# Kernel tuning notes

Measured on AMD Instinct MI355X. Metric: run time of the kernel, lower is better.

The kernel has to match this reference:

```python
import jax, jax.numpy as jnp
import numpy as np

C, H, W = 3, 128, 128
N_PIX = C * H * W            # 49152
N_RET = N_PIX // 16          # 3072
N_LGN = N_RET                # 3072
N_V1 = 2 * N_RET             # 6144
N_IT = N_RET                 # 3072
N_CLS = 1000
BATCH = 256


def setup_inputs() -> dict:
    key = jax.random.key(0)
    ks = jax.random.split(key, 14)
    x = jax.random.normal(ks[0], (BATCH, C, H, W), dtype=jnp.float32)
    w_ret = jax.random.normal(ks[1], (N_RET, 16), dtype=jnp.float32) * 0.1
    b_ret = jax.random.normal(ks[2], (N_RET,), dtype=jnp.float32) * 0.1
    w_lgn = jax.random.normal(ks[3], (N_LGN, 16), dtype=jnp.float32) * 0.1
    b_lgn = jax.random.normal(ks[4], (N_LGN,), dtype=jnp.float32) * 0.1
    w_v1 = jax.random.normal(ks[5], (N_V1, 32), dtype=jnp.float32) * 0.1
    b_v1 = jax.random.normal(ks[6], (N_V1,), dtype=jnp.float32) * 0.1
    w_it = jax.random.normal(ks[7], (N_IT, 32), dtype=jnp.float32) * 0.1
    b_it = jax.random.normal(ks[8], (N_IT,), dtype=jnp.float32) * 0.1
    W_cls = jax.random.normal(ks[9], (N_CLS, N_IT), dtype=jnp.float32) * 0.02
    b_cls = jnp.zeros((N_CLS,), dtype=jnp.float32)
    # pixel_map: arange(n_pixels) tiled/truncated to (n_retina, 16); here exact reshape
    pixel_map = jnp.arange(N_PIX, dtype=jnp.int32).reshape(N_RET, 16)
    m1 = jax.random.bernoulli(ks[10], 0.01, (N_V1, N_LGN)).astype(jnp.int32)
    m1 = m1.at[jnp.arange(N_V1), jnp.arange(N_V1) % N_LGN].set(1)
    m2 = jax.random.bernoulli(ks[11], 0.01, (N_IT, N_V1)).astype(jnp.int32)
    m2 = m2.at[jnp.arange(N_IT), jnp.arange(N_IT) % N_V1].set(1)
    return {"x": x, "w_ret": w_ret, "b_ret": b_ret, "w_lgn": w_lgn, "b_lgn": b_lgn,
            "w_v1": w_v1, "b_v1": b_v1, "w_it": w_it, "b_it": b_it,
            "W_cls": W_cls, "b_cls": b_cls, "pixel_map": pixel_map,
            "lgn_to_v1": m1, "v1_to_it": m2}


def reference(x, w_ret, b_ret, w_lgn, b_lgn, w_v1, b_v1, w_it, b_it,
              W_cls, b_cls, pixel_map, lgn_to_v1, v1_to_it):
    B = x.shape[0]
    x_flat = x.reshape(B, -1)                                  # [B, n_pix]
    # Retina: per-neuron gather of 16-pixel receptive field, then spike
    pix = x_flat[:, pixel_map.reshape(-1)].reshape(B, N_RET, 16)  # [B, n_ret, 16]
    r1 = jax.nn.sigmoid(jnp.einsum('bnk,nk->bn', pix, w_ret) - b_ret)
    # LGN: scalar input broadcast over the 4x4 field -> scalar * sum(w)
    r2 = jax.nn.sigmoid(r1 * jnp.sum(w_lgn, axis=1) - b_lgn)
    # V1: mean over sparse LGN neighborhood, broadcast over 4x8 field
    m1 = lgn_to_v1.astype(r2.dtype)                             # [n_v1, n_lgn]
    v1_in = (r2 @ m1.T) / jnp.sum(m1, axis=1)                   # [B, n_v1]
    r3 = jax.nn.sigmoid(v1_in * jnp.sum(w_v1, axis=1) - b_v1)
    # IT: mean over sparse V1 neighborhood
    m2 = v1_to_it.astype(r3.dtype)                              # [n_it, n_v1]
    it_in = (r3 @ m2.T) / jnp.sum(m2, axis=1)                   # [B, n_it]
    r4 = jax.nn.sigmoid(it_in * jnp.sum(w_it, axis=1) - b_it)
    return r4 @ W_cls.T + b_cls                                 # [B, n_classes]
```

## Files before the change

kernel.cpp:

```cpp
#include <hip/hip_runtime.h>

#define B     256
#define NPIX  49152
#define NRET  3072
#define NV1   6144
#define NIT   3072
#define NCLS  1000

#define CC      8
#define SPLITK  8
#define KCH     (NIT / SPLITK)

__device__ __forceinline__ float sigmoidf_(float v) {
    return 1.0f / (1.0f + __expf(-v));
}

__global__ __launch_bounds__(256) void k_retina(
    const float* __restrict__ x, const float* __restrict__ w_ret,
    const float* __restrict__ b_ret, const float* __restrict__ w_lgn,
    const float* __restrict__ b_lgn, const int* __restrict__ pixel_map,
    float* __restrict__ r2)
{
    int b = blockIdx.y;
    int n = blockIdx.x * 256 + threadIdx.x;
    const float* xb = x + (size_t)b * NPIX;
    const int4*   pm4 = (const int4*)(pixel_map + n * 16);
    const float4* wr4 = (const float4*)(w_ret + n * 16);
    const float4* wl4 = (const float4*)(w_lgn + n * 16);
    float dot = 0.f, sl = 0.f;
#pragma unroll
    for (int q = 0; q < 4; ++q) {
        int4 p = pm4[q];
        float4 w = wr4[q];
        dot += xb[p.x] * w.x + xb[p.y] * w.y + xb[p.z] * w.z + xb[p.w] * w.w;
        float4 l = wl4[q];
        sl += l.x + l.y + l.z + l.w;
    }
    float r1 = sigmoidf_(dot - b_ret[n]);
    r2[(size_t)b * NRET + n] = sigmoidf_(r1 * sl - b_lgn[n]);
}

__global__ __launch_bounds__(256) void k_transpose(
    const float* __restrict__ in, float* __restrict__ out)
{
    __shared__ float tile[32][33];
    int tx = threadIdx.x & 31, ty = threadIdx.x >> 5;
    int n0 = blockIdx.x * 32, b0 = blockIdx.y * 32;
#pragma unroll
    for (int i = 0; i < 4; ++i)
        tile[ty + i * 8][tx] = in[(size_t)(b0 + ty + i * 8) * NRET + n0 + tx];
    __syncthreads();
#pragma unroll
    for (int i = 0; i < 4; ++i)
        out[(size_t)(n0 + ty + i * 8) * B + b0 + tx] = tile[tx][ty + i * 8];
}

template<int K>
__global__ __launch_bounds__(256) void k_sparse(
    const float* __restrict__ act_t,
    const int*   __restrict__ mask,
    const float* __restrict__ w,
    const float* __restrict__ bias,
    float*       __restrict__ out_t)
{
    __shared__ int   idxs[1024];
    __shared__ int   cnt;
    __shared__ float wrow[32];
    int j = blockIdx.x;
    int t = threadIdx.x;
    if (t == 0) cnt = 0;
    if (t < 32) wrow[t] = w[j * 32 + t];
    __syncthreads();

    const int4* row4 = (const int4*)(mask + (size_t)j * K);
    for (int q = t; q < K / 4; q += 256) {
        int4 m = row4[q];
        int base = q * 4;
        if (m.x) { int p = atomicAdd(&cnt, 1); if (p < 1024) idxs[p] = base;     }
        if (m.y) { int p = atomicAdd(&cnt, 1); if (p < 1024) idxs[p] = base + 1; }
        if (m.z) { int p = atomicAdd(&cnt, 1); if (p < 1024) idxs[p] = base + 2; }
        if (m.w) { int p = atomicAdd(&cnt, 1); if (p < 1024) idxs[p] = base + 3; }
    }
    __syncthreads();

    int n = cnt < 1024 ? cnt : 1024;
    float acc = 0.f;
    for (int i = 0; i < n; ++i)
        acc += act_t[(size_t)idxs[i] * B + t];

    float sw = 0.f;
#pragma unroll
    for (int i = 0; i < 32; ++i) sw += wrow[i];

    float v = acc / (float)n * sw - bias[j];
    out_t[(size_t)j * B + t] = sigmoidf_(v);
}

__global__ __launch_bounds__(256) void k_cls(
    const float* __restrict__ r4t,
    const float* __restrict__ W,
    float*       __restrict__ part)
{
    __shared__ float wl[CC * KCH];
    int c0 = blockIdx.x * CC;
    int ky = blockIdx.y;
    int k0 = ky * KCH;
    int t  = threadIdx.x;
#pragma unroll
    for (int c = 0; c < CC; ++c)
        for (int kk = t; kk < KCH; kk += 256)
            wl[c * KCH + kk] = W[(size_t)(c0 + c) * NIT + k0 + kk];
    __syncthreads();

    float acc[CC];
#pragma unroll
    for (int c = 0; c < CC; ++c) acc[c] = 0.f;

    const float4* wl4 = (const float4*)wl;
    for (int kk = 0; kk < KCH; kk += 4) {
        float4 r;
        r.x = r4t[(size_t)(k0 + kk    ) * B + t];
        r.y = r4t[(size_t)(k0 + kk + 1) * B + t];
        r.z = r4t[(size_t)(k0 + kk + 2) * B + t];
        r.w = r4t[(size_t)(k0 + kk + 3) * B + t];
#pragma unroll
        for (int c = 0; c < CC; ++c) {
            float4 w = wl4[(c * KCH + kk) >> 2];
            acc[c] += r.x * w.x + r.y * w.y + r.z * w.z + r.w * w.w;
        }
    }
    float* dst = part + (size_t)ky * (B * NCLS) + (size_t)t * NCLS + c0;
#pragma unroll
    for (int c = 0; c < CC; ++c) dst[c] = acc[c];
}

__global__ __launch_bounds__(256) void k_cls_reduce(
    const float* __restrict__ part, const float* __restrict__ b_cls,
    float* __restrict__ out)
{
    int i = blockIdx.x * 256 + threadIdx.x;
    float s = b_cls[i % NCLS];
#pragma unroll
    for (int p = 0; p < SPLITK; ++p) s += part[(size_t)p * (B * NCLS) + i];
    out[i] = s;
}

extern "C" void kernel_launch(void* const* d_in, const int* in_sizes, int n_in,
                              void* d_out, int out_size, void* d_ws, size_t ws_size,
                              hipStream_t stream) {
    const float* x      = (const float*)d_in[0];
    const float* w_ret  = (const float*)d_in[1];
    const float* b_ret  = (const float*)d_in[2];
    const float* w_lgn  = (const float*)d_in[3];
    const float* b_lgn  = (const float*)d_in[4];
    const float* w_v1   = (const float*)d_in[5];
    const float* b_v1   = (const float*)d_in[6];
    const float* w_it   = (const float*)d_in[7];
    const float* b_it   = (const float*)d_in[8];
    const float* W_cls  = (const float*)d_in[9];
    const float* b_cls  = (const float*)d_in[10];
    const int*   pixmap = (const int*)d_in[11];
    const int*   m1     = (const int*)d_in[12];
    const int*   m2     = (const int*)d_in[13];
    float* out = (float*)d_out;

    float* ws  = (float*)d_ws;
    float* r2   = ws;
    float* r2t  = r2  + (size_t)B * NRET;
    float* r3t  = r2t + (size_t)NRET * B;
    float* r4t  = r3t + (size_t)NV1 * B;
    float* part = r4t + (size_t)NIT * B;

    k_retina<<<dim3(NRET / 256, B), 256, 0, stream>>>(x, w_ret, b_ret, w_lgn, b_lgn, pixmap, r2);
    k_transpose<<<dim3(NRET / 32, B / 32), 256, 0, stream>>>(r2, r2t);
    k_sparse<NRET><<<NV1, 256, 0, stream>>>(r2t, m1, w_v1, b_v1, r3t);
    k_sparse<NV1><<<NIT, 256, 0, stream>>>(r3t, m2, w_it, b_it, r4t);
    k_cls<<<dim3(NCLS / CC, SPLITK), 256, 0, stream>>>(r4t, W_cls, part);
    k_cls_reduce<<<(B * NCLS) / 256, 256, 0, stream>>>(part, b_cls, out);
}
```

Before: 334.0 us.

## Fuse retina with transpose, wave-per-row sparse kernels, bf16 MFMA classifier

```diff
diff --git a/kernel.cpp b/kernel.cpp
--- a/kernel.cpp
+++ b/kernel.cpp
@@ -7,141 +7,208 @@
 #define NIT   3072
 #define NCLS  1000
 
-#define CC      8
-#define SPLITK  8
-#define KCH     (NIT / SPLITK)
+typedef unsigned short ushort_t;
+typedef __bf16 bf16x8 __attribute__((ext_vector_type(8)));
+typedef float  f32x4  __attribute__((ext_vector_type(4)));
 
 __device__ __forceinline__ float sigmoidf_(float v) {
     return 1.0f / (1.0f + __expf(-v));
 }
 
-__global__ __launch_bounds__(256) void k_retina(
+__device__ __forceinline__ ushort_t f2bf(float f) {
+    union { float f; unsigned u; } v; v.f = f;
+    unsigned r = (v.u + 0x7fffu + ((v.u >> 16) & 1u)) >> 16;
+    return (ushort_t)r;
+}
+
+__global__ __launch_bounds__(256) void k_retina_t(
     const float* __restrict__ x, const float* __restrict__ w_ret,
     const float* __restrict__ b_ret, const float* __restrict__ w_lgn,
     const float* __restrict__ b_lgn, const int* __restrict__ pixel_map,
-    float* __restrict__ r2)
-{
-    int b = blockIdx.y;
-    int n = blockIdx.x * 256 + threadIdx.x;
-    const float* xb = x + (size_t)b * NPIX;
+    float* __restrict__ r2t)
+{
+    __shared__ float tile[32][33];
+    int tx = threadIdx.x & 31, ty = threadIdx.x >> 5;
+    int n0 = blockIdx.x * 32, b0 = blockIdx.y * 32;
+    int n = n0 + tx;
     const int4*   pm4 = (const int4*)(pixel_map + n * 16);
     const float4* wr4 = (const float4*)(w_ret + n * 16);
     const float4* wl4 = (const float4*)(w_lgn + n * 16);
-    float dot = 0.f, sl = 0.f;
+    int4 p[4]; float4 wr[4]; float slw = 0.f;
 #pragma unroll
     for (int q = 0; q < 4; ++q) {
-        int4 p = pm4[q];
-        float4 w = wr4[q];
-        dot += xb[p.x] * w.x + xb[p.y] * w.y + xb[p.z] * w.z + xb[p.w] * w.w;
-        float4 l = wl4[q];
-        sl += l.x + l.y + l.z + l.w;
-    }
-    float r1 = sigmoidf_(dot - b_ret[n]);
-    r2[(size_t)b * NRET + n] = sigmoidf_(r1 * sl - b_lgn[n]);
-}
-
-__global__ __launch_bounds__(256) void k_transpose(
-    const float* __restrict__ in, float* __restrict__ out)
-{
-    __shared__ float tile[32][33];
-    int tx = threadIdx.x & 31, ty = threadIdx.x >> 5;
-    int n0 = blockIdx.x * 32, b0 = blockIdx.y * 32;
+        p[q] = pm4[q]; wr[q] = wr4[q];
+        float4 L = wl4[q]; slw += L.x + L.y + L.z + L.w;
+    }
+    float br = b_ret[n], bl = b_lgn[n];
+#pragma unroll
+    for (int i = 0; i < 4; ++i) {
+        int b = b0 + ty + i * 8;
+        const float* xb = x + (size_t)b * NPIX;
+        float dot = 0.f;
+#pragma unroll
+        for (int q = 0; q < 4; ++q)
+            dot += xb[p[q].x] * wr[q].x + xb[p[q].y] * wr[q].y
+                 + xb[p[q].z] * wr[q].z + xb[p[q].w] * wr[q].w;
+        float r1 = sigmoidf_(dot - br);
+        tile[ty + i * 8][tx] = sigmoidf_(r1 * slw - bl);
+    }
+    __syncthreads();
 #pragma unroll
     for (int i = 0; i < 4; ++i)
-        tile[ty + i * 8][tx] = in[(size_t)(b0 + ty + i * 8) * NRET + n0 + tx];
-    __syncthreads();
-#pragma unroll
-    for (int i = 0; i < 4; ++i)
-        out[(size_t)(n0 + ty + i * 8) * B + b0 + tx] = tile[tx][ty + i * 8];
-}
-
-template<int K>
+        r2t[(size_t)(n0 + ty + i * 8) * B + b0 + tx] = tile[tx][ty + i * 8];
+}
+
+template<int K, bool OUT_BF16>
 __global__ __launch_bounds__(256) void k_sparse(
     const float* __restrict__ act_t,
     const int*   __restrict__ mask,
     const float* __restrict__ w,
     const float* __restrict__ bias,
-    float*       __restrict__ out_t)
-{
-    __shared__ int   idxs[1024];
-    __shared__ int   cnt;
-    __shared__ float wrow[32];
-    int j = blockIdx.x;
-    int t = threadIdx.x;
-    if (t == 0) cnt = 0;
-    if (t < 32) wrow[t] = w[j * 32 + t];
-    __syncthreads();
+    void*        __restrict__ out_t)
+{
+    constexpr int MAXI = 192;
+    __shared__ int idxs[4][MAXI];
+    __shared__ int cnts[4];
+    int t = threadIdx.x, wv = t >> 6, l = t & 63;
+    int j = blockIdx.x * 4 + wv;
+    if (l == 0) cnts[wv] = 0;
 
     const int4* row4 = (const int4*)(mask + (size_t)j * K);
-    for (int q = t; q < K / 4; q += 256) {
+#pragma unroll
+    for (int q = l; q < K / 4; q += 64) {
         int4 m = row4[q];
         int base = q * 4;
-        if (m.x) { int p = atomicAdd(&cnt, 1); if (p < 1024) idxs[p] = base;     }
-        if (m.y) { int p = atomicAdd(&cnt, 1); if (p < 1024) idxs[p] = base + 1; }
-        if (m.z) { int p = atomicAdd(&cnt, 1); if (p < 1024) idxs[p] = base + 2; }
-        if (m.w) { int p = atomicAdd(&cnt, 1); if (p < 1024) idxs[p] = base + 3; }
-    }
-    __syncthreads();
-
-    int n = cnt < 1024 ? cnt : 1024;
-    float acc = 0.f;
-    for (int i = 0; i < n; ++i)
-        acc += act_t[(size_t)idxs[i] * B + t];
-
-    float sw = 0.f;
-#pragma unroll
-    for (int i = 0; i < 32; ++i) sw += wrow[i];
-
-    float v = acc / (float)n * sw - bias[j];
-    out_t[(size_t)j * B + t] = sigmoidf_(v);
-}
-
-__global__ __launch_bounds__(256) void k_cls(
-    const float* __restrict__ r4t,
+        if (m.x) { int p = atomicAdd(&cnts[wv], 1); if (p < MAXI) idxs[wv][p] = base;     }
+        if (m.y) { int p = atomicAdd(&cnts[wv], 1); if (p < MAXI) idxs[wv][p] = base + 1; }
+        if (m.z) { int p = atomicAdd(&cnts[wv], 1); if (p < MAXI) idxs[wv][p] = base + 2; }
+        if (m.w) { int p = atomicAdd(&cnts[wv], 1); if (p < MAXI) idxs[wv][p] = base + 3; }
+    }
+    int n = cnts[wv];
+    if (n > MAXI) n = MAXI;
+
+    const float4* a4 = (const float4*)act_t;
+    float4 acc0 = {0,0,0,0}, acc1 = {0,0,0,0};
+    int i = 0;
+    for (; i + 2 <= n; i += 2) {
+        int j0 = idxs[wv][i], j1 = idxs[wv][i + 1];
+        float4 v0 = a4[(size_t)j0 * 64 + l];
+        float4 v1 = a4[(size_t)j1 * 64 + l];
+        acc0.x += v0.x; acc0.y += v0.y; acc0.z += v0.z; acc0.w += v0.w;
+        acc1.x += v1.x; acc1.y += v1.y; acc1.z += v1.z; acc1.w += v1.w;
+    }
+    if (i < n) {
+        float4 v0 = a4[(size_t)idxs[wv][i] * 64 + l];
+        acc0.x += v0.x; acc0.y += v0.y; acc0.z += v0.z; acc0.w += v0.w;
+    }
+    acc0.x += acc1.x; acc0.y += acc1.y; acc0.z += acc1.z; acc0.w += acc1.w;
+
+    float sw = w[(size_t)j * 32 + (l & 31)];
+#pragma unroll
+    for (int off = 1; off < 32; off <<= 1) sw += __shfl_xor(sw, off);
+
+    float bj = bias[j];
+    float scale = sw / (float)n;
+    float o0 = sigmoidf_(acc0.x * scale - bj);
+    float o1 = sigmoidf_(acc0.y * scale - bj);
+    float o2 = sigmoidf_(acc0.z * scale - bj);
+    float o3 = sigmoidf_(acc0.w * scale - bj);
+
+    if (OUT_BF16) {
+        ushort_t* dst = (ushort_t*)out_t + (size_t)j * B + l * 4;
+        ushort4 o; o.x = f2bf(o0); o.y = f2bf(o1); o.z = f2bf(o2); o.w = f2bf(o3);
+        *(ushort4*)dst = o;
+    } else {
+        float4* dst = (float4*)((float*)out_t + (size_t)j * B + l * 4);
+        float4 o; o.x = o0; o.y = o1; o.z = o2; o.w = o3;
+        *dst = o;
+    }
+}
+
+__global__ __launch_bounds__(256) void k_prep(
     const float* __restrict__ W,
-    float*       __restrict__ part)
-{
-    __shared__ float wl[CC * KCH];
-    int c0 = blockIdx.x * CC;
-    int ky = blockIdx.y;
-    int k0 = ky * KCH;
-    int t  = threadIdx.x;
-#pragma unroll
-    for (int c = 0; c < CC; ++c)
-        for (int kk = t; kk < KCH; kk += 256)
-            wl[c * KCH + kk] = W[(size_t)(c0 + c) * NIT + k0 + kk];
-    __syncthreads();
-
-    float acc[CC];
-#pragma unroll
-    for (int c = 0; c < CC; ++c) acc[c] = 0.f;
-
-    const float4* wl4 = (const float4*)wl;
-    for (int kk = 0; kk < KCH; kk += 4) {
-        float4 r;
-        r.x = r4t[(size_t)(k0 + kk    ) * B + t];
-        r.y = r4t[(size_t)(k0 + kk + 1) * B + t];
-        r.z = r4t[(size_t)(k0 + kk + 2) * B + t];
-        r.w = r4t[(size_t)(k0 + kk + 3) * B + t];
-#pragma unroll
-        for (int c = 0; c < CC; ++c) {
-            float4 w = wl4[(c * KCH + kk) >> 2];
-            acc[c] += r.x * w.x + r.y * w.y + r.z * w.z + r.w * w.w;
+    const ushort_t* __restrict__ r4bt,
+    ushort_t* __restrict__ wbf,
+    ushort_t* __restrict__ r4b)
+{
+    __shared__ ushort_t stile[32][33];
+    int bx = blockIdx.x, t = threadIdx.x;
+    if (bx < 1536) {
+        int e = (bx * 256 + t) * 8;
+        uint4 o = {0, 0, 0, 0};
+        if (e < NCLS * NIT) {
+            float4 f0 = *(const float4*)(W + e);
+            float4 f1 = *(const float4*)(W + e + 4);
+            o.x = (unsigned)f2bf(f0.x) | ((unsigned)f2bf(f0.y) << 16);
+            o.y = (unsigned)f2bf(f0.z) | ((unsigned)f2bf(f0.w) << 16);
+            o.z = (unsigned)f2bf(f1.x) | ((unsigned)f2bf(f1.y) << 16);
+            o.w = (unsigned)f2bf(f1.z) | ((unsigned)f2bf(f1.w) << 16);
         }
-    }
-    float* dst = part + (size_t)ky * (B * NCLS) + (size_t)t * NCLS + c0;
-#pragma unroll
-    for (int c = 0; c < CC; ++c) dst[c] = acc[c];
-}
-
-__global__ __launch_bounds__(256) void k_cls_reduce(
+        *(uint4*)(wbf + e) = o;
+    } else {
+        int tb = bx - 1536;
+        int tn = tb / 8, tbb = tb % 8;
+        int tx = t & 31, ty = t >> 5;
+#pragma unroll
+        for (int i = 0; i < 4; ++i)
+            stile[ty + i * 8][tx] = r4bt[(size_t)(tn * 32 + ty + i * 8) * B + tbb * 32 + tx];
+        __syncthreads();
+#pragma unroll
+        for (int i = 0; i < 4; ++i)
+            r4b[(size_t)(tbb * 32 + ty + i * 8) * NIT + tn * 32 + tx] = stile[tx][ty + i * 8];
+    }
+}
+
+__global__ __launch_bounds__(256) void k_cls_mfma(
+    const ushort_t* __restrict__ r4b,
+    const ushort_t* __restrict__ wbf,
+    float* __restrict__ part)
+{
+    int t = threadIdx.x, wv = t >> 6, l = t & 63;
+    int cb = blockIdx.x, bb = blockIdx.y, kz = blockIdx.z;
+    int m = l & 15, quad = l >> 4;
+    int brow = bb * 64 + wv * 16 + m;
+    const bf16x8* pa = (const bf16x8*)(r4b + (size_t)brow * NIT + kz * 768 + quad * 8);
+    const bf16x8* pb0 = (const bf16x8*)(wbf + (size_t)(cb * 64 +  0 + m) * NIT + kz * 768 + quad * 8);
+    const bf16x8* pb1 = (const bf16x8*)(wbf + (size_t)(cb * 64 + 16 + m) * NIT + kz * 768 + quad * 8);
+    const bf16x8* pb2 = (const bf16x8*)(wbf + (size_t)(cb * 64 + 32 + m) * NIT + kz * 768 + quad * 8);
+    const bf16x8* pb3 = (const bf16x8*)(wbf + (size_t)(cb * 64 + 48 + m) * NIT + kz * 768 + quad * 8);
+
+    f32x4 acc0 = {0,0,0,0}, acc1 = {0,0,0,0}, acc2 = {0,0,0,0}, acc3 = {0,0,0,0};
+#pragma unroll 4
+    for (int s = 0; s < 24; ++s) {
+        bf16x8 a  = pa [s * 4];
+        bf16x8 b0 = pb0[s * 4];
+        bf16x8 b1 = pb1[s * 4];
+        bf16x8 b2 = pb2[s * 4];
+        bf16x8 b3 = pb3[s * 4];
+        acc0 = __builtin_amdgcn_mfma_f32_16x16x32_bf16(a, b0, acc0, 0, 0, 0);
+        acc1 = __builtin_amdgcn_mfma_f32_16x16x32_bf16(a, b1, acc1, 0, 0, 0);
+        acc2 = __builtin_amdgcn_mfma_f32_16x16x32_bf16(a, b2, acc2, 0, 0, 0);
+        acc3 = __builtin_amdgcn_mfma_f32_16x16x32_bf16(a, b3, acc3, 0, 0, 0);
+    }
+    float* dst = part + (size_t)kz * (B * NCLS);
+    int rb = bb * 64 + wv * 16 + quad * 4;
+#pragma unroll
+    for (int ct = 0; ct < 4; ++ct) {
+        f32x4 a = ct == 0 ? acc0 : ct == 1 ? acc1 : ct == 2 ? acc2 : acc3;
+        int c = cb * 64 + ct * 16 + m;
+        if (c < NCLS) {
+#pragma unroll
+            for (int r = 0; r < 4; ++r)
+                dst[(size_t)(rb + r) * NCLS + c] = a[r];
+        }
+    }
+}
+
+__global__ __launch_bounds__(256) void k_reduce(
     const float* __restrict__ part, const float* __restrict__ b_cls,
     float* __restrict__ out)
 {
     int i = blockIdx.x * 256 + threadIdx.x;
     float s = b_cls[i % NCLS];
 #pragma unroll
-    for (int p = 0; p < SPLITK; ++p) s += part[(size_t)p * (B * NCLS) + i];
+    for (int z = 0; z < 4; ++z) s += part[(size_t)z * (B * NCLS) + i];
     out[i] = s;
 }
 
@@ -164,17 +231,19 @@
     const int*   m2     = (const int*)d_in[13];
     float* out = (float*)d_out;
 
-    float* ws  = (float*)d_ws;
-    float* r2   = ws;
-    float* r2t  = r2  + (size_t)B * NRET;
-    float* r3t  = r2t + (size_t)NRET * B;
-    float* r4t  = r3t + (size_t)NV1 * B;
-    float* part = r4t + (size_t)NIT * B;
-
-    k_retina<<<dim3(NRET / 256, B), 256, 0, stream>>>(x, w_ret, b_ret, w_lgn, b_lgn, pixmap, r2);
-    k_transpose<<<dim3(NRET / 32, B / 32), 256, 0, stream>>>(r2, r2t);
-    k_sparse<NRET><<<NV1, 256, 0, stream>>>(r2t, m1, w_v1, b_v1, r3t);
-    k_sparse<NV1><<<NIT, 256, 0, stream>>>(r3t, m2, w_it, b_it, r4t);
-    k_cls<<<dim3(NCLS / CC, SPLITK), 256, 0, stream>>>(r4t, W_cls, part);
-    k_cls_reduce<<<(B * NCLS) / 256, 256, 0, stream>>>(part, b_cls, out);
-}
+    char* w = (char*)d_ws;
+    float*    r2t  = (float*)(w);
+    float*    r3t  = (float*)(w +  3145728);
+    ushort_t* r4bt = (ushort_t*)(w +  9437184);
+    ushort_t* r4b  = (ushort_t*)(w + 11010048);
+    ushort_t* wbf  = (ushort_t*)(w + 12582912);
+    float*    part = (float*)(w + 18874368);
+
+    k_retina_t<<<dim3(NRET / 32, B / 32), 256, 0, stream>>>(
+        x, w_ret, b_ret, w_lgn, b_lgn, pixmap, r2t);
+    k_sparse<NRET, false><<<NV1 / 4, 256, 0, stream>>>(r2t, m1, w_v1, b_v1, r3t);
+    k_sparse<NV1, true><<<NIT / 4, 256, 0, stream>>>(r3t, m2, w_it, b_it, r4bt);
+    k_prep<<<2304, 256, 0, stream>>>(W_cls, r4bt, wbf, r4b);
+    k_cls_mfma<<<dim3(16, 4, 4), 256, 0, stream>>>(r4b, wbf, part);
+    k_reduce<<<(B * NCLS) / 256, 256, 0, stream>>>(part, b_cls, out);
+}
```

New measurement: 301.9 us. -9.6%, faster.
